# Optimization experiments

Hardware: AMD Instinct MI355X
Metric: run time of the kernel (lower is better)

Reference implementation:

```python
import jax, jax.numpy as jnp
import numpy as np

N_NODES = 32000
N_EDGES = 512000
F_IN = 128
HEADS = 4
CH = 64
NODES_PER_GRAPH = 500
BATCH = 64
HID = 512
ZDIM = 64


def _gat_layer(x, src, dst, W, att_src, att_dst, bias):
    # PyG GATConv, concat=True, negative_slope=0.2, self-loops already appended.
    N = x.shape[0]
    h = (x @ W).reshape(N, HEADS, CH)                 # [N,H,C]
    a_s = jnp.sum(h * att_src, axis=-1)               # [N,H]
    a_d = jnp.sum(h * att_dst, axis=-1)               # [N,H]
    e = jax.nn.leaky_relu(a_s[src] + a_d[dst], negative_slope=0.2)  # [E,H]
    m = jax.ops.segment_max(e, dst, num_segments=N)   # segment softmax over dst
    p = jnp.exp(e - m[dst])
    denom = jax.ops.segment_sum(p, dst, num_segments=N)
    alpha = p / denom[dst]                            # [E,H]
    out = jax.ops.segment_sum(h[src] * alpha[..., None], dst, num_segments=N)
    return out.reshape(N, HEADS * CH) + bias


def setup_inputs() -> dict:
    key = jax.random.key(0)
    ks = jax.random.split(key, 16)
    s = 0.02
    x = jax.random.normal(ks[0], (N_NODES, F_IN), jnp.float32)
    edge_index = jax.random.randint(ks[1], (2, N_EDGES), 0, N_NODES, jnp.int64)
    W1 = jax.random.normal(ks[2], (F_IN, HEADS * CH), jnp.float32) * s
    att_src1 = jax.random.normal(ks[3], (HEADS, CH), jnp.float32) * s
    att_dst1 = jax.random.normal(ks[4], (HEADS, CH), jnp.float32) * s
    b1 = jnp.zeros((HEADS * CH,), jnp.float32)
    W2 = jax.random.normal(ks[5], (HEADS * CH, HEADS * CH), jnp.float32) * s
    att_src2 = jax.random.normal(ks[6], (HEADS, CH), jnp.float32) * s
    att_dst2 = jax.random.normal(ks[7], (HEADS, CH), jnp.float32) * s
    b2 = jnp.zeros((HEADS * CH,), jnp.float32)
    We = jax.random.normal(ks[8], (NODES_PER_GRAPH * HEADS * CH, HID), jnp.float32) * 0.002
    be = jnp.zeros((HID,), jnp.float32)
    Wmu = jax.random.normal(ks[9], (HID, ZDIM), jnp.float32) * s
    bmu = jnp.zeros((ZDIM,), jnp.float32)
    Wvar = jax.random.normal(ks[10], (HID, ZDIM), jnp.float32) * s
    bvar = jnp.zeros((ZDIM,), jnp.float32)
    return {"x": x, "W1": W1, "att_src1": att_src1, "att_dst1": att_dst1, "b1": b1,
            "W2": W2, "att_src2": att_src2, "att_dst2": att_dst2, "b2": b2,
            "We": We, "be": be, "Wmu": Wmu, "bmu": bmu, "Wvar": Wvar, "bvar": bvar,
            "edge_index": edge_index, "batch": BATCH}


def reference(x, W1, att_src1, att_dst1, b1, W2, att_src2, att_dst2, b2,
              We, be, Wmu, bmu, Wvar, bvar, edge_index, batch):
    N = x.shape[0]
    loops = jnp.arange(N, dtype=edge_index.dtype)
    src = jnp.concatenate([edge_index[0], loops])
    dst = jnp.concatenate([edge_index[1], loops])
    h = jax.nn.relu(_gat_layer(x, src, dst, W1, att_src1, att_dst1, b1))
    h = jax.nn.relu(_gat_layer(h, src, dst, W2, att_src2, att_dst2, b2))
    xg = h.reshape(batch, -1)                         # [B, in_fea*H*C]
    y = xg @ We + be                                  # [B, HID]
    mu_b = jnp.mean(y, axis=0)                        # BatchNorm1d (training stats), eps=1e-3
    var_b = jnp.var(y, axis=0)
    y = (y - mu_b) / jnp.sqrt(var_b + 1e-3)
    mu_l = jnp.mean(y, axis=-1, keepdims=True)        # LayerNorm, no affine, eps=1e-5
    var_l = jnp.var(y, axis=-1, keepdims=True)
    y = (y - mu_l) / jnp.sqrt(var_l + 1e-5)
    y = jax.nn.relu(y)
    z_loc = y @ Wmu + bmu
    z_scale = jnp.exp(y @ Wvar + bvar) + 1e-4
    return (z_loc, z_scale)
```

## Files before the change

### kernel.cpp

```cpp
#include <hip/hip_runtime.h>
#include <math.h>

#define NN 32000
#define FIN 128
#define HC 256
#define NH 4
#define HIDD 512
#define BB 64
#define ZD 64
#define NSPLIT 125
#define KBCH 1024
#define BNB 128

typedef __bf16 bf16x8 __attribute__((ext_vector_type(8)));
typedef float f32x4 __attribute__((ext_vector_type(4)));
typedef unsigned int uint;

__device__ inline float lrelu(float x){ return x > 0.f ? x : 0.2f*x; }
__device__ inline unsigned short f2b(float f){
  uint u = __float_as_uint(f);
  return (unsigned short)((u + 0x7FFFu + ((u >> 16) & 1u)) >> 16);
}
__device__ inline float b2f(unsigned short b){ return __uint_as_float(((uint)b) << 16); }
__device__ inline float blo(uint v){ return __uint_as_float(v << 16); }
__device__ inline float bhi(uint v){ return __uint_as_float(v & 0xffff0000u); }
__device__ inline uint cvtpk(float lo, float hi){
  uint pk;
  asm("v_cvt_pk_bf16_f32 %0, %1, %2" : "=v"(pk) : "v"(lo), "v"(hi));
  return pk;
}

__global__ void k_prep0(const void* ei, int* flag, int* counts){
  int b = blockIdx.x, t = threadIdx.x;
  if (b == 0 && t < 64){
    int v = ((const int*)ei)[2*t + 1];
    unsigned long long bal = __ballot(v == 0);
    if (t == 0) *flag = (bal == ~0ULL) ? 1 : 0;
  }
  for (int i = b*256 + t; i < NN; i += gridDim.x*256) counts[i] = 0;
}

__global__ void k_prep1(const float* __restrict__ x, unsigned short* __restrict__ xb,
                        const float* __restrict__ W1, unsigned short* __restrict__ Wt1,
                        const float* __restrict__ W2, unsigned short* __restrict__ Wt2,
                        const void* ei, const int* __restrict__ flag,
                        int* __restrict__ counts, int E){
  int b = blockIdx.x, t = threadIdx.x;
  if (b < 4000){
    int i = b*1024 + t*4;
    float4 v = *(const float4*)&x[i];
    uint p0 = cvtpk(v.x, v.y), p1 = cvtpk(v.z, v.w);
    uint2 o; o.x = p0; o.y = p1;
    *(uint2*)&xb[i] = o;
  } else if (b < 4512){
    int bb = b - 4000;
    int n = bb & 255, which = bb >> 8;
    if (which == 0){ if (t < FIN) Wt1[n*FIN + t] = f2b(W1[t*HC + n]); }
    else           { Wt2[n*HC + t] = f2b(W2[t*HC + n]); }
  } else {
    int i = (b - 4512)*256 + t;
    if (i < E){
      int d = *flag ? (int)((const long long*)ei)[E + i] : ((const int*)ei)[E + i];
      atomicAdd(&counts[d], 1);
    }
  }
}

__global__ __launch_bounds__(256) void k_scanA(const int* __restrict__ counts,
                                               int* __restrict__ bsum){
  __shared__ int red[256];
  int b = blockIdx.x, t = threadIdx.x;
  red[t] = counts[b*256 + t];
  __syncthreads();
  #pragma unroll
  for (int o = 128; o; o >>= 1){
    if (t < o) red[t] += red[t + o];
    __syncthreads();
  }
  if (t == 0) bsum[b] = red[0];
}

__global__ __launch_bounds__(128) void k_scanB(int* __restrict__ bsum, int nb){
  __shared__ int s[128];
  int t = threadIdx.x;
  int v = (t < nb) ? bsum[t] : 0;
  s[t] = v;
  __syncthreads();
  for (int o = 1; o < 128; o <<= 1){
    int u = (t >= o) ? s[t - o] : 0;
    __syncthreads();
    s[t] += u;
    __syncthreads();
  }
  if (t < nb) bsum[t] = s[t] - v;
}

__global__ __launch_bounds__(256) void k_scanC(const int* __restrict__ counts,
    const int* __restrict__ bsum, int* __restrict__ offs, int* __restrict__ cursor){
  __shared__ int s[256];
  int b = blockIdx.x, t = threadIdx.x;
  int v = counts[b*256 + t];
  s[t] = v;
  __syncthreads();
  for (int o = 1; o < 256; o <<= 1){
    int u = (t >= o) ? s[t - o] : 0;
    __syncthreads();
    s[t] += u;
    __syncthreads();
  }
  int excl = s[t] - v + bsum[b];
  offs[b*256 + t] = excl;
  cursor[b*256 + t] = excl;
  if (b == (NN/256 - 1) && t == 255) offs[NN] = excl + v;
}

__global__ void k_fill(const void* ei, const int* __restrict__ flag,
                       int* __restrict__ cursor, int* __restrict__ col, int E){
  int i = blockIdx.x*256 + threadIdx.x;
  if (i < E){
    int s, d;
    if (*flag){ s = (int)((const long long*)ei)[i]; d = (int)((const long long*)ei)[E + i]; }
    else      { s = ((const int*)ei)[i];            d = ((const int*)ei)[E + i]; }
    int pos = atomicAdd(&cursor[d], 1);
    col[pos] = s;
  }
}

__global__ __launch_bounds__(256) void k_gemm_n(const unsigned short* __restrict__ A,
    const unsigned short* __restrict__ Wt, int K,
    const float* __restrict__ ws, const float* __restrict__ wd,
    unsigned short* __restrict__ out, float* __restrict__ a_s, float* __restrict__ a_d){
  __shared__ unsigned short As[2][64][40];
  __shared__ unsigned short Bs[2][256][40];
  int m0 = blockIdx.x * 64;
  int t = threadIdx.x;
  int w = t >> 6, lane = t & 63, l15 = lane & 15, l16 = lane >> 4;
  int arow = t >> 2, ako = (t & 3) * 8;
  const unsigned short* aptr = A + (size_t)(m0 + arow)*K + ako;
  const unsigned short* bptr = Wt + (size_t)t*K;
  f32x4 acc[16];
  #pragma unroll
  for (int c = 0; c < 16; c++) acc[c] = (f32x4){0.f,0.f,0.f,0.f};

  uint4 a4 = *(const uint4*)aptr;
  uint4 b4[4];
  #pragma unroll
  for (int p = 0; p < 4; p++) b4[p] = *(const uint4*)(bptr + p*8);

  int pp = 0;
  for (int k0 = 0; k0 < K; k0 += 32){
    *(uint4*)&As[pp][arow][ako] = a4;
    #pragma unroll
    for (int p = 0; p < 4; p++) *(uint4*)&Bs[pp][t][p*8] = b4[p];
    __syncthreads();
    if (k0 + 32 < K){
      a4 = *(const uint4*)(aptr + k0 + 32);
      #pragma unroll
      for (int p = 0; p < 4; p++) b4[p] = *(const uint4*)(bptr + k0 + 32 + p*8);
    }
    bf16x8 af = *(const bf16x8*)&As[pp][w*16 + l15][l16*8];
    #pragma unroll
    for (int c = 0; c < 16; c++){
      bf16x8 bfr = *(const bf16x8*)&Bs[pp][c*16 + l15][l16*8];
      acc[c] = __builtin_amdgcn_mfma_f32_16x16x32_bf16(af, bfr, acc[c], 0, 0, 0);
    }
    pp ^= 1;
  }

  #pragma unroll
  for (int r = 0; r < 4; r++){
    int row = m0 + w*16 + l16*4 + r;
    float hs[NH] = {0,0,0,0}, hd[NH] = {0,0,0,0};
    #pragma unroll
    for (int c = 0; c < 16; c++){
      float v = acc[c][r];
      int colc = c*16 + l15;
      out[(size_t)row*HC + colc] = f2b(v);
      hs[c>>2] += v * ws[colc];
      hd[c>>2] += v * wd[colc];
    }
    #pragma unroll
    for (int h = 0; h < NH; h++){
      float s = hs[h], d = hd[h];
      #pragma unroll
      for (int o = 1; o < 16; o <<= 1){ s += __shfl_xor(s, o); d += __shfl_xor(d, o); }
      if (l15 == h){ a_s[row*NH + h] = s; a_d[row*NH + h] = d; }
    }
  }
}

__global__ __launch_bounds__(256) void k_agg(const unsigned short* __restrict__ hp,
    const int* __restrict__ col, const int* __restrict__ offs,
    const float* __restrict__ a_s, const float* __restrict__ a_d,
    const float* __restrict__ bias, unsigned short* __restrict__ outb){
  int n = blockIdx.x*4 + (threadIdx.x >> 6);
  int lane = threadIdx.x & 63;
  int g = lane >> 4, l16 = lane & 15;
  int h = l16 >> 2;
  int c0 = l16 * 16;
  int b0 = offs[n], b1 = offs[n+1];
  float adh = a_d[n*NH + h];
  float pself = expf(lrelu(a_s[n*NH + h] + adh));
  float den = 0.f;
  float ac[16];
  #pragma unroll
  for (int j = 0; j < 16; j++) ac[j] = 0.f;
  #pragma unroll 2
  for (int i = b0 + g; i < b1; i += 4){
    int s = col[i];
    float p = expf(lrelu(a_s[s*NH + h] + adh));
    den += p;
    uint4 v0 = *(const uint4*)&hp[(size_t)s*HC + c0];
    uint4 v1 = *(const uint4*)&hp[(size_t)s*HC + c0 + 8];
    ac[0] = fmaf(p, blo(v0.x), ac[0]);   ac[1] = fmaf(p, bhi(v0.x), ac[1]);
    ac[2] = fmaf(p, blo(v0.y), ac[2]);   ac[3] = fmaf(p, bhi(v0.y), ac[3]);
    ac[4] = fmaf(p, blo(v0.z), ac[4]);   ac[5] = fmaf(p, bhi(v0.z), ac[5]);
    ac[6] = fmaf(p, blo(v0.w), ac[6]);   ac[7] = fmaf(p, bhi(v0.w), ac[7]);
    ac[8] = fmaf(p, blo(v1.x), ac[8]);   ac[9] = fmaf(p, bhi(v1.x), ac[9]);
    ac[10]= fmaf(p, blo(v1.y), ac[10]);  ac[11]= fmaf(p, bhi(v1.y), ac[11]);
    ac[12]= fmaf(p, blo(v1.z), ac[12]);  ac[13]= fmaf(p, bhi(v1.z), ac[13]);
    ac[14]= fmaf(p, blo(v1.w), ac[14]);  ac[15]= fmaf(p, bhi(v1.w), ac[15]);
  }
  den += __shfl_xor(den, 16);  den += __shfl_xor(den, 32);
  #pragma unroll
  for (int j = 0; j < 16; j++){
    ac[j] += __shfl_xor(ac[j], 16);
    ac[j] += __shfl_xor(ac[j], 32);
  }
  den += pself;
  float r = 1.f / den;
  if (g == 0){
    uint4 hv0 = *(const uint4*)&hp[(size_t)n*HC + c0];
    uint4 hv1 = *(const uint4*)&hp[(size_t)n*HC + c0 + 8];
    float hvf[16] = {blo(hv0.x),bhi(hv0.x),blo(hv0.y),bhi(hv0.y),
                     blo(hv0.z),bhi(hv0.z),blo(hv0.w),bhi(hv0.w),
                     blo(hv1.x),bhi(hv1.x),blo(hv1.y),bhi(hv1.y),
                     blo(hv1.z),bhi(hv1.z),blo(hv1.w),bhi(hv1.w)};
    uint ov[8];
    #pragma unroll
    for (int j = 0; j < 8; j++){
      float e0 = fmaxf((pself*hvf[2*j]   + ac[2*j]  )*r + bias[c0+2*j],   0.f);
      float e1 = fmaxf((pself*hvf[2*j+1] + ac[2*j+1])*r + bias[c0+2*j+1], 0.f);
      ov[j] = ((uint)f2b(e1) << 16) | (uint)f2b(e0);
    }
    *(uint4*)&outb[(size_t)n*HC + c0]     = *(uint4*)&ov[0];
    *(uint4*)&outb[(size_t)n*HC + c0 + 8] = *(uint4*)&ov[4];
  }
}

__global__ __launch_bounds__(256) void k_gemm_big(const unsigned short* __restrict__ xg,
    const float* __restrict__ We, float* __restrict__ part){
  __shared__ unsigned short As[2][64][40];
  __shared__ unsigned short Bs[2][BNB][40];
  int n0 = blockIdx.x * BNB;
  int kc = blockIdx.y;
  int kbase = kc * KBCH;
  int t = threadIdx.x, w = t >> 6, lane = t & 63, l15 = lane & 15, l16 = lane >> 4;
  int cc = t & (BNB-1);
  int khalf = t >> 7;
  int arow = t >> 2, ako = (t & 3) * 8;
  const float* bptr = We + (size_t)(kbase + khalf*16)*HIDD + n0 + cc;
  const unsigned short* aptr = xg + (size_t)arow*128000 + kbase + ako;
  f32x4 acc[8];
  #pragma unroll
  for (int c = 0; c < 8; c++) acc[c] = (f32x4){0.f,0.f,0.f,0.f};

  float rv[16]; uint4 a4;
  #pragma unroll
  for (int mm = 0; mm < 16; mm++) rv[mm] = bptr[(size_t)mm*HIDD];
  a4 = *(const uint4*)aptr;

  int p = 0;
  for (int ks = 0; ks < KBCH; ks += 32){
    *(uint4*)&As[p][arow][ako] = a4;
    #pragma unroll
    for (int j = 0; j < 8; j++)
      *(uint*)&Bs[p][cc][khalf*16 + 2*j] = cvtpk(rv[2*j], rv[2*j+1]);
    __syncthreads();
    if (ks + 32 < KBCH){
      const float* bp2 = bptr + (size_t)(ks + 32)*HIDD;
      #pragma unroll
      for (int mm = 0; mm < 16; mm++) rv[mm] = bp2[(size_t)mm*HIDD];
      a4 = *(const uint4*)(aptr + ks + 32);
    }
    bf16x8 af = *(const bf16x8*)&As[p][w*16 + l15][l16*8];
    #pragma unroll
    for (int c = 0; c < 8; c++){
      bf16x8 bfr = *(const bf16x8*)&Bs[p][c*16 + l15][l16*8];
      acc[c] = __builtin_amdgcn_mfma_f32_16x16x32_bf16(af, bfr, acc[c], 0, 0, 0);
    }
    p ^= 1;
  }
  float* pbase = part + (size_t)kc*BB*HIDD;
  #pragma unroll
  for (int r = 0; r < 4; r++){
    int row = w*16 + l16*4 + r;
    #pragma unroll
    for (int c = 0; c < 8; c++)
      pbase[row*HIDD + n0 + c*16 + l15] = acc[c][r];
  }
}

__global__ void k_reduce(const float* __restrict__ part, const float* __restrict__ be,
                         float* __restrict__ y){
  int o = blockIdx.x*256 + threadIdx.x;
  float s = 0.f;
  #pragma unroll 5
  for (int k = 0; k < NSPLIT; k++) s += part[(size_t)k*BB*HIDD + o];
  y[o] = s + be[o & (HIDD-1)];
}

__global__ __launch_bounds__(64) void k_bn(const float* __restrict__ y,
    float* __restrict__ ybn){
  int colb = blockIdx.x, r = threadIdx.x;
  float v = y[(size_t)r*HIDD + colb];
  float s = v, s2 = v*v;
  #pragma unroll
  for (int o = 32; o; o >>= 1){ s += __shfl_down(s, o); s2 += __shfl_down(s2, o); }
  s = __shfl(s, 0); s2 = __shfl(s2, 0);
  float mean = s * (1.f/BB);
  float var = s2 * (1.f/BB) - mean*mean;
  ybn[(size_t)r*HIDD + colb] = (v - mean) * rsqrtf(var + 1e-3f);
}

__global__ __launch_bounds__(512) void k_lnheads(const float* __restrict__ ybn,
    const float* __restrict__ Wmu, const float* __restrict__ bmu,
    const float* __restrict__ Wvar, const float* __restrict__ bvar,
    float* __restrict__ out){
  __shared__ float ssum[8], ssq[8];
  __shared__ float yrow[HIDD];
  int row = blockIdx.x, t = threadIdx.x;
  float v = ybn[(size_t)row*HIDD + t];
  float s = v, s2 = v*v;
  #pragma unroll
  for (int o = 32; o; o >>= 1){ s += __shfl_down(s, o); s2 += __shfl_down(s2, o); }
  if ((t & 63) == 0){ ssum[t>>6] = s; ssq[t>>6] = s2; }
  __syncthreads();
  if (t == 0){
    float S = 0, S2 = 0;
    for (int i = 0; i < 8; i++){ S += ssum[i]; S2 += ssq[i]; }
    ssum[0] = S; ssq[0] = S2;
  }
  __syncthreads();
  float mean = ssum[0] * (1.f/HIDD);
  float var = ssq[0] * (1.f/HIDD) - mean*mean;
  yrow[t] = fmaxf((v - mean) * rsqrtf(var + 1e-5f), 0.f);
  __syncthreads();
  int o = t >> 2, kq = t & 3;
  const float* Wc = (o < ZD) ? Wmu : Wvar;
  int j = (o < ZD) ? o : o - ZD;
  float acc = 0.f;
  #pragma unroll 4
  for (int k = kq*128; k < kq*128 + 128; k++)
    acc = fmaf(yrow[k], Wc[(size_t)k*ZD + j], acc);
  acc += __shfl_down(acc, 1);
  acc += __shfl_down(acc, 2);
  if (kq == 0){
    if (o < ZD) out[row*ZD + o] = acc + bmu[o];
    else        out[BB*ZD + row*ZD + j] = expf(acc + bvar[j]) + 1e-4f;
  }
}

extern "C" void kernel_launch(void* const* d_in, const int* in_sizes, int n_in,
                              void* d_out, int out_size, void* d_ws, size_t ws_size,
                              hipStream_t stream){
  const float* x    = (const float*)d_in[0];
  const float* W1   = (const float*)d_in[1];
  const float* as1  = (const float*)d_in[2];
  const float* ad1  = (const float*)d_in[3];
  const float* b1   = (const float*)d_in[4];
  const float* W2   = (const float*)d_in[5];
  const float* as2  = (const float*)d_in[6];
  const float* ad2  = (const float*)d_in[7];
  const float* b2   = (const float*)d_in[8];
  const float* We   = (const float*)d_in[9];
  const float* be   = (const float*)d_in[10];
  const float* Wmu  = (const float*)d_in[11];
  const float* bmu  = (const float*)d_in[12];
  const float* Wvar = (const float*)d_in[13];
  const float* bvar = (const float*)d_in[14];
  const void*  ei   = d_in[15];
  int E = in_sizes[15] / 2;

  char* w = (char*)d_ws;
  auto alloc = [&](size_t bytes)->void*{
    void* p = (void*)w; w += (bytes + 255) & ~(size_t)255; return p;
  };
  unsigned short* gb   = (unsigned short*)alloc((size_t)NN*HC*2);
  unsigned short* ab   = (unsigned short*)alloc((size_t)NN*HC*2);
  unsigned short* xb   = (unsigned short*)alloc((size_t)NN*FIN*2);
  unsigned short* Wt1  = (unsigned short*)alloc((size_t)HC*FIN*2);
  unsigned short* Wt2  = (unsigned short*)alloc((size_t)HC*HC*2);
  float*    a_s    = (float*)alloc((size_t)NN*NH*4);
  float*    a_d    = (float*)alloc((size_t)NN*NH*4);
  int*      counts = (int*)alloc((size_t)NN*4);
  int*      offs   = (int*)alloc((size_t)(NN+1)*4);
  int*      cursor = (int*)alloc((size_t)NN*4);
  int*      col    = (int*)alloc((size_t)E*4);
  int*      bsum   = (int*)alloc((size_t)256*4);
  int*      flag   = (int*)alloc(256);
  float*    part   = (float*)alloc((size_t)NSPLIT*BB*HIDD*4);
  float*    y      = (float*)alloc((size_t)BB*HIDD*4);
  float*    ybn    = (float*)alloc((size_t)BB*HIDD*4);

  k_prep0<<<125, 256, 0, stream>>>(ei, flag, counts);
  k_prep1<<<4512 + (E + 255)/256, 256, 0, stream>>>(x, xb, W1, Wt1, W2, Wt2,
                                                    ei, flag, counts, E);
  k_scanA<<<NN/256, 256, 0, stream>>>(counts, bsum);
  k_scanB<<<1, 128, 0, stream>>>(bsum, NN/256);
  k_scanC<<<NN/256, 256, 0, stream>>>(counts, bsum, offs, cursor);
  k_fill<<<(E + 255)/256, 256, 0, stream>>>(ei, flag, cursor, col, E);

  k_gemm_n<<<NN/64, 256, 0, stream>>>(xb, Wt1, FIN, as1, ad1, gb, a_s, a_d);
  k_agg<<<NN/4, 256, 0, stream>>>(gb, col, offs, a_s, a_d, b1, ab);

  k_gemm_n<<<NN/64, 256, 0, stream>>>(ab, Wt2, HC, as2, ad2, gb, a_s, a_d);
  k_agg<<<NN/4, 256, 0, stream>>>(gb, col, offs, a_s, a_d, b2, ab);

  k_gemm_big<<<dim3(HIDD/BNB, NSPLIT), 256, 0, stream>>>(ab, We, part);
  k_reduce<<<BB*HIDD/256, 256, 0, stream>>>(part, be, y);
  k_bn<<<HIDD, 64, 0, stream>>>(y, ybn);
  k_lnheads<<<BB, 512, 0, stream>>>(ybn, Wmu, bmu, Wvar, bvar, (float*)d_out);
}
```

Baseline: 288.5 us.

## Fuse scan stages, merge CSR fill into first GEMM, replace split-K reduce with atomics

Removes the single-block scanB kernel: each scanC block now sums the preceding block totals itself. The CSR fill pass moves into extra blocks of the first node GEMM, so both run in one launch. The split-K partial buffer and its reduce kernel are replaced by float atomicAdd into a zeroed y, and the encoder bias is dropped because the training-mode BatchNorm that follows cancels it. The aim is fewer launches and no 16 MB partial write/read, at the cost of 125-way atomic contention per output and a non-deterministic summation order.

```diff
diff --git a/kernel.cpp b/kernel.cpp
--- a/kernel.cpp
+++ b/kernel.cpp
@@ -80,25 +80,20 @@
   if (t == 0) bsum[b] = red[0];
 }
 
-__global__ __launch_bounds__(128) void k_scanB(int* __restrict__ bsum, int nb){
-  __shared__ int s[128];
-  int t = threadIdx.x;
-  int v = (t < nb) ? bsum[t] : 0;
-  s[t] = v;
-  __syncthreads();
-  for (int o = 1; o < 128; o <<= 1){
-    int u = (t >= o) ? s[t - o] : 0;
-    __syncthreads();
-    s[t] += u;
-    __syncthreads();
-  }
-  if (t < nb) bsum[t] = s[t] - v;
-}
-
 __global__ __launch_bounds__(256) void k_scanC(const int* __restrict__ counts,
     const int* __restrict__ bsum, int* __restrict__ offs, int* __restrict__ cursor){
   __shared__ int s[256];
   int b = blockIdx.x, t = threadIdx.x;
+  int bv = (t < b) ? bsum[t] : 0;
+  s[t] = bv;
+  __syncthreads();
+  #pragma unroll
+  for (int o = 128; o; o >>= 1){
+    if (t < o) s[t] += s[t + o];
+    __syncthreads();
+  }
+  int base = s[0];
+  __syncthreads();
   int v = counts[b*256 + t];
   s[t] = v;
   __syncthreads();
@@ -108,31 +103,19 @@
     s[t] += u;
     __syncthreads();
   }
-  int excl = s[t] - v + bsum[b];
+  int excl = s[t] - v + base;
   offs[b*256 + t] = excl;
   cursor[b*256 + t] = excl;
   if (b == (NN/256 - 1) && t == 255) offs[NN] = excl + v;
 }
 
-__global__ void k_fill(const void* ei, const int* __restrict__ flag,
-                       int* __restrict__ cursor, int* __restrict__ col, int E){
-  int i = blockIdx.x*256 + threadIdx.x;
-  if (i < E){
-    int s, d;
-    if (*flag){ s = (int)((const long long*)ei)[i]; d = (int)((const long long*)ei)[E + i]; }
-    else      { s = ((const int*)ei)[i];            d = ((const int*)ei)[E + i]; }
-    int pos = atomicAdd(&cursor[d], 1);
-    col[pos] = s;
-  }
-}
-
-__global__ __launch_bounds__(256) void k_gemm_n(const unsigned short* __restrict__ A,
+__device__ __forceinline__ void gemm_n_body(const unsigned short* __restrict__ A,
     const unsigned short* __restrict__ Wt, int K,
     const float* __restrict__ ws, const float* __restrict__ wd,
-    unsigned short* __restrict__ out, float* __restrict__ a_s, float* __restrict__ a_d){
+    unsigned short* __restrict__ out, float* __restrict__ a_s, float* __restrict__ a_d,
+    int m0){
   __shared__ unsigned short As[2][64][40];
   __shared__ unsigned short Bs[2][256][40];
-  int m0 = blockIdx.x * 64;
   int t = threadIdx.x;
   int w = t >> 6, lane = t & 63, l15 = lane & 15, l16 = lane >> 4;
   int arow = t >> 2, ako = (t & 3) * 8;
@@ -185,6 +168,33 @@
       #pragma unroll
       for (int o = 1; o < 16; o <<= 1){ s += __shfl_xor(s, o); d += __shfl_xor(d, o); }
       if (l15 == h){ a_s[row*NH + h] = s; a_d[row*NH + h] = d; }
+    }
+  }
+}
+
+__global__ __launch_bounds__(256) void k_gemm_n(const unsigned short* __restrict__ A,
+    const unsigned short* __restrict__ Wt, int K,
+    const float* __restrict__ ws, const float* __restrict__ wd,
+    unsigned short* __restrict__ out, float* __restrict__ a_s, float* __restrict__ a_d){
+  gemm_n_body(A, Wt, K, ws, wd, out, a_s, a_d, blockIdx.x * 64);
+}
+
+__global__ __launch_bounds__(256) void k_gemm1f(const unsigned short* __restrict__ A,
+    const unsigned short* __restrict__ Wt, int K,
+    const float* __restrict__ ws, const float* __restrict__ wd,
+    unsigned short* __restrict__ out, float* __restrict__ a_s, float* __restrict__ a_d,
+    const void* ei, const int* __restrict__ flag,
+    int* __restrict__ cursor, int* __restrict__ col, int E){
+  if (blockIdx.x < NN/64){
+    gemm_n_body(A, Wt, K, ws, wd, out, a_s, a_d, blockIdx.x * 64);
+  } else {
+    int i = (blockIdx.x - NN/64)*256 + threadIdx.x;
+    if (i < E){
+      int s, d;
+      if (*flag){ s = (int)((const long long*)ei)[i]; d = (int)((const long long*)ei)[E + i]; }
+      else      { s = ((const int*)ei)[i];            d = ((const int*)ei)[E + i]; }
+      int pos = atomicAdd(&cursor[d], 1);
+      col[pos] = s;
     }
   }
 }
@@ -249,7 +259,7 @@
 }
 
 __global__ __launch_bounds__(256) void k_gemm_big(const unsigned short* __restrict__ xg,
-    const float* __restrict__ We, float* __restrict__ part){
+    const float* __restrict__ We, float* __restrict__ y){
   __shared__ unsigned short As[2][64][40];
   __shared__ unsigned short Bs[2][BNB][40];
   int n0 = blockIdx.x * BNB;
@@ -291,23 +301,13 @@
     }
     p ^= 1;
   }
-  float* pbase = part + (size_t)kc*BB*HIDD;
   #pragma unroll
   for (int r = 0; r < 4; r++){
     int row = w*16 + l16*4 + r;
     #pragma unroll
     for (int c = 0; c < 8; c++)
-      pbase[row*HIDD + n0 + c*16 + l15] = acc[c][r];
-  }
-}
-
-__global__ void k_reduce(const float* __restrict__ part, const float* __restrict__ be,
-                         float* __restrict__ y){
-  int o = blockIdx.x*256 + threadIdx.x;
-  float s = 0.f;
-  #pragma unroll 5
-  for (int k = 0; k < NSPLIT; k++) s += part[(size_t)k*BB*HIDD + o];
-  y[o] = s + be[o & (HIDD-1)];
+      atomicAdd(&y[row*HIDD + n0 + c*16 + l15], acc[c][r]);
+  }
 }
 
 __global__ __launch_bounds__(64) void k_bn(const float* __restrict__ y,
@@ -374,7 +374,6 @@
   const float* ad2  = (const float*)d_in[7];
   const float* b2   = (const float*)d_in[8];
   const float* We   = (const float*)d_in[9];
-  const float* be   = (const float*)d_in[10];
   const float* Wmu  = (const float*)d_in[11];
   const float* bmu  = (const float*)d_in[12];
   const float* Wvar = (const float*)d_in[13];
@@ -399,26 +398,26 @@
   int*      col    = (int*)alloc((size_t)E*4);
   int*      bsum   = (int*)alloc((size_t)256*4);
   int*      flag   = (int*)alloc(256);
-  float*    part   = (float*)alloc((size_t)NSPLIT*BB*HIDD*4);
   float*    y      = (float*)alloc((size_t)BB*HIDD*4);
   float*    ybn    = (float*)alloc((size_t)BB*HIDD*4);
 
+  int nfill = (E + 255)/256;
+
   k_prep0<<<125, 256, 0, stream>>>(ei, flag, counts);
-  k_prep1<<<4512 + (E + 255)/256, 256, 0, stream>>>(x, xb, W1, Wt1, W2, Wt2,
-                                                    ei, flag, counts, E);
+  k_prep1<<<4512 + nfill, 256, 0, stream>>>(x, xb, W1, Wt1, W2, Wt2,
+                                            ei, flag, counts, E);
   k_scanA<<<NN/256, 256, 0, stream>>>(counts, bsum);
-  k_scanB<<<1, 128, 0, stream>>>(bsum, NN/256);
   k_scanC<<<NN/256, 256, 0, stream>>>(counts, bsum, offs, cursor);
-  k_fill<<<(E + 255)/256, 256, 0, stream>>>(ei, flag, cursor, col, E);
-
-  k_gemm_n<<<NN/64, 256, 0, stream>>>(xb, Wt1, FIN, as1, ad1, gb, a_s, a_d);
+
+  k_gemm1f<<<NN/64 + nfill, 256, 0, stream>>>(xb, Wt1, FIN, as1, ad1, gb, a_s, a_d,
+                                              ei, flag, cursor, col, E);
   k_agg<<<NN/4, 256, 0, stream>>>(gb, col, offs, a_s, a_d, b1, ab);
 
   k_gemm_n<<<NN/64, 256, 0, stream>>>(ab, Wt2, HC, as2, ad2, gb, a_s, a_d);
   k_agg<<<NN/4, 256, 0, stream>>>(gb, col, offs, a_s, a_d, b2, ab);
 
-  k_gemm_big<<<dim3(HIDD/BNB, NSPLIT), 256, 0, stream>>>(ab, We, part);
-  k_reduce<<<BB*HIDD/256, 256, 0, stream>>>(part, be, y);
+  hipMemsetAsync(y, 0, (size_t)BB*HIDD*4, stream);
+  k_gemm_big<<<dim3(HIDD/BNB, NSPLIT), 256, 0, stream>>>(ab, We, y);
   k_bn<<<HIDD, 64, 0, stream>>>(y, ybn);
   k_lnheads<<<BB, 512, 0, stream>>>(ybn, Wmu, bmu, Wvar, bvar, (float*)d_out);
 }
```

Measured after the change: 291.7 us. About the same (+1.1%).
